# Optimization experiments

Measured on AMD Instinct MI355X. Metric: run time of the kernel, lower is better.

The kernel has to match this reference:

```python
import jax, jax.numpy as jnp
import numpy as np

N = 100000
E = 1600000
IN_F = 128
OUT_F = 64
NEG_SLOPE = 0.2


def setup_inputs() -> dict:
    key = jax.random.key(0)
    k1, k2, k3, k4 = jax.random.split(key, 4)
    h = jax.random.normal(k1, (N, IN_F), dtype=jnp.float32)
    edge_index = jax.random.randint(k2, (2, E), 0, N, dtype=jnp.int64 if jax.config.jax_enable_x64 else jnp.int32)
    # glorot-initialized params (scale ~ sqrt(6/(fan_in+fan_out)))
    ws = float(np.sqrt(6.0 / (IN_F + OUT_F)))
    W = jax.random.uniform(k3, (OUT_F, IN_F), dtype=jnp.float32, minval=-ws, maxval=ws)
    as_ = float(np.sqrt(6.0 / (1 + 2 * OUT_F)))
    a = jax.random.uniform(k4, (1, 2 * OUT_F), dtype=jnp.float32, minval=-as_, maxval=as_)
    return {"h": h, "W": W, "a": a, "edge_index": edge_index}


def reference(h, W, a, edge_index):
    n = h.shape[0]
    f_out = W.shape[0]
    h_lin = h @ W.T  # [N, F_out]
    # add self loops
    loops = jnp.arange(n, dtype=edge_index.dtype)
    row = jnp.concatenate([edge_index[0], loops])  # [E+N]
    col = jnp.concatenate([edge_index[1], loops])
    # cat([h_lin[row], h_lin[col]]) @ a.T == h_lin[row]@a1 + h_lin[col]@a2
    a1 = a[0, :f_out]
    a2 = a[0, f_out:]
    s_src = h_lin @ a1  # [N]
    s_dst = h_lin @ a2  # [N]
    e = s_src[row] + s_dst[col]  # [E+N]
    e = jnp.where(e > 0, e, NEG_SLOPE * e)  # LeakyReLU
    # segment softmax over destination (row); every row appears via self loop
    m = jax.ops.segment_max(e, row, num_segments=n)
    ex = jnp.exp(e - m[row])
    denom = jax.ops.segment_sum(ex, row, num_segments=n)
    alpha = ex / denom[row]
    # scatter-add aggregation
    h_prime = jax.ops.segment_sum(alpha[:, None] * h_lin[col], row, num_segments=n)
    return jax.nn.elu(h_prime)
```

## Files before the change

### kernel.cpp

```cpp
#include <hip/hip_runtime.h>
#include <cstdint>

#define N_NODES 100000
#define E_EDGES 1600000
#define TOTAL_E (E_EDGES + N_NODES)
#define IN_F 128
#define OUT_F 64
#define NEG_SLOPE 0.2f

#define NB   256
#define RPB  391
#define GCAP 8192
#define TILE 4096
#define EPT  (TILE / 256)
#define HALF_R 196
#define CCAP 4608

typedef __attribute__((ext_vector_type(8))) short short8;
typedef __attribute__((ext_vector_type(4))) float float4v;

__device__ __forceinline__ short bf16_rne(float x) {
  unsigned u = __builtin_bit_cast(unsigned, x);
  unsigned r = u + 0x7FFFu + ((u >> 16) & 1u);
  return (short)(r >> 16);
}
__device__ __forceinline__ float bf16_f(short s) {
  unsigned u = ((unsigned)(unsigned short)s) << 16;
  return __builtin_bit_cast(float, u);
}
__device__ __forceinline__ float bf16u_f(unsigned short s) {
  unsigned u = ((unsigned)s) << 16;
  return __builtin_bit_cast(float, u);
}

__global__ __launch_bounds__(256) void k_linear(
    const float* __restrict__ h, const float* __restrict__ W,
    const float* __restrict__ a, unsigned short* __restrict__ h_lin,
    float* __restrict__ s_src, float* __restrict__ s_dst) {
  __shared__ alignas(16) short Whi[16 * 512];
  __shared__ alignas(16) short Wlo[16 * 512];

  const int tid = threadIdx.x;
  for (int i = tid; i < OUT_F * IN_F; i += 256) {
    const int n = i >> 7, k = i & 127;
    const float x = W[i];
    const short hi = bf16_rne(x);
    const short lo = bf16_rne(x - bf16_f(hi));
    const int idx = (((k >> 5) * 4 + (n >> 4)) << 9) |
                    (((((k >> 3) & 3) << 4) | (n & 15)) << 3) | (k & 7);
    Whi[idx] = hi;
    Wlo[idx] = lo;
  }
  __syncthreads();

  const int lane = tid & 63;
  const int m    = lane & 15;
  const int q    = lane >> 4;
  const int wgid = blockIdx.x * 4 + (tid >> 6);
  const int nw   = gridDim.x * 4;

  float a1v[4], a2v[4];
#pragma unroll
  for (int t = 0; t < 4; ++t) {
    a1v[t] = a[t * 16 + m];
    a2v[t] = a[OUT_F + t * 16 + m];
  }

  for (int tile = wgid; tile < N_NODES / 16; tile += nw) {
    const int row0 = tile * 16;
    float4v acc[4] = {{0.f,0.f,0.f,0.f},{0.f,0.f,0.f,0.f},
                      {0.f,0.f,0.f,0.f},{0.f,0.f,0.f,0.f}};

    const float* hbase = h + (size_t)(row0 + m) * IN_F + q * 8;
#pragma unroll
    for (int ks = 0; ks < 4; ++ks) {
      const float4 f0 = *(const float4*)(hbase + 32 * ks);
      const float4 f1 = *(const float4*)(hbase + 32 * ks + 4);
      float av[8] = {f0.x, f0.y, f0.z, f0.w, f1.x, f1.y, f1.z, f1.w};
      short8 ahi, alo;
#pragma unroll
      for (int j = 0; j < 8; ++j) {
        const short hi = bf16_rne(av[j]);
        ahi[j] = hi;
        alo[j] = bf16_rne(av[j] - bf16_f(hi));
      }
#pragma unroll
      for (int t = 0; t < 4; ++t) {
        const int fb = ((ks * 4 + t) << 9) + lane * 8;
        const short8 bhi = *(const short8*)&Whi[fb];
        const short8 blo = *(const short8*)&Wlo[fb];
        acc[t] = __builtin_amdgcn_mfma_f32_16x16x32_bf16(ahi, bhi, acc[t], 0, 0, 0);
        acc[t] = __builtin_amdgcn_mfma_f32_16x16x32_bf16(ahi, blo, acc[t], 0, 0, 0);
        acc[t] = __builtin_amdgcn_mfma_f32_16x16x32_bf16(alo, bhi, acc[t], 0, 0, 0);
      }
    }

#pragma unroll
    for (int t = 0; t < 4; ++t)
#pragma unroll
      for (int r = 0; r < 4; ++r)
        h_lin[(size_t)(row0 + q * 4 + r) * OUT_F + t * 16 + m] =
            (unsigned short)bf16_rne(acc[t][r]);

#pragma unroll
    for (int r = 0; r < 4; ++r) {
      float p = acc[0][r] * a1v[0] + acc[1][r] * a1v[1] +
                acc[2][r] * a1v[2] + acc[3][r] * a1v[3];
      float qq = acc[0][r] * a2v[0] + acc[1][r] * a2v[1] +
                 acc[2][r] * a2v[2] + acc[3][r] * a2v[3];
#pragma unroll
      for (int o = 1; o < 16; o <<= 1) {
        p  += __shfl_xor(p, o, 64);
        qq += __shfl_xor(qq, o, 64);
      }
      if (m == 0) {
        s_src[row0 + q * 4 + r] = p;
        s_dst[row0 + q * 4 + r] = qq;
      }
    }
  }
}

__global__ __launch_bounds__(256) void k_bin(
    const int* __restrict__ ei, int* __restrict__ gcur,
    unsigned* __restrict__ regions) {
  __shared__ unsigned reord[TILE];
  __shared__ unsigned char bktid[TILE];
  __shared__ int hist[NB];
  __shared__ int scan_s[NB];
  __shared__ int adj[NB];
  __shared__ int wsum[4];

  const int tid = threadIdx.x;
  const int e0  = blockIdx.x * TILE;

  hist[tid] = 0;
  __syncthreads();

  int      myb[EPT];
  unsigned myrec[EPT];
#pragma unroll
  for (int k = 0; k < EPT; ++k) {
    const int e = e0 + k * 256 + tid;
    int b = -1; unsigned rec = 0;
    if (e < TOTAL_E) {
      int r, c;
      if (e < E_EDGES) { r = ei[e]; c = ei[E_EDGES + e]; }
      else             { r = e - E_EDGES; c = r; }
      b = (int)((unsigned)r / RPB);
      rec = ((unsigned)(r - b * RPB) << 17) | (unsigned)c;
      atomicAdd(&hist[b], 1);
    }
    myb[k] = b; myrec[k] = rec;
  }
  __syncthreads();

  const int lane = tid & 63, w = tid >> 6;
  {
    const int v = hist[tid];
    int incl = v;
#pragma unroll
    for (int o = 1; o < 64; o <<= 1) {
      const int t = __shfl_up(incl, o, 64);
      if (lane >= o) incl += t;
    }
    if (lane == 63) wsum[w] = incl;
    __syncthreads();
    int wpre = 0;
    for (int i = 0; i < w; ++i) wpre += wsum[i];
    scan_s[tid] = wpre + incl - v;
    adj[tid]    = wpre + incl - v;
  }
  __syncthreads();

#pragma unroll
  for (int k = 0; k < EPT; ++k) {
    if (myb[k] >= 0) {
      const int pos = atomicAdd(&adj[myb[k]], 1);
      reord[pos]  = myrec[k];
      bktid[pos]  = (unsigned char)myb[k];
    }
  }
  __syncthreads();

  {
    const int cnt = hist[tid];
    int a2 = 0;
    if (cnt > 0) a2 = atomicAdd(&gcur[tid], cnt) - scan_s[tid];
    __syncthreads();
    adj[tid] = a2;
  }
  __syncthreads();

  const int tilesz = scan_s[NB - 1] + hist[NB - 1];
  for (int i = tid; i < tilesz; i += 256) {
    const int b    = bktid[i];
    const int slot = adj[b] + i;
    if (slot < GCAP) regions[(size_t)b * GCAP + slot] = reord[i];
  }
}

__global__ __launch_bounds__(1024) void k_agg(
    const unsigned short* __restrict__ h_lin, const float* __restrict__ s_src,
    const float* __restrict__ s_dst, const int* __restrict__ gcur,
    const unsigned* __restrict__ regions, float* __restrict__ out) {
  __shared__ int cnt[HALF_R];
  __shared__ int off[HALF_R];
  __shared__ int cols[CCAP];
  __shared__ int wsum4[4];

  const int blk  = blockIdx.x;
  const int b    = blk >> 1;
  const int half = blk & 1;
  const int rlo  = half * HALF_R;
  const int hr   = half ? (RPB - HALF_R) : HALF_R;
  const int tid  = threadIdx.x;
  const int row0 = b * RPB + rlo;
  const int m    = min(gcur[b], GCAP);
  const unsigned* reg = regions + (size_t)b * GCAP;

  for (int i = tid; i < HALF_R; i += 1024) cnt[i] = 0;
  __syncthreads();

  unsigned myrec[GCAP / 1024];
  int nmy = 0;
  for (int i = tid; i < m; i += 1024) {
    const unsigned rec = reg[i];
    const int rl = (int)(rec >> 17) - rlo;
    if (rl >= 0 && rl < hr) {
      myrec[nmy++] = rec;
      atomicAdd(&cnt[rl], 1);
    }
  }
  __syncthreads();

  const int lane = tid & 63, wv = tid >> 6;
  int incl = 0, v = 0;
  if (tid < 256) {
    v = (tid < hr) ? cnt[tid] : 0;
    incl = v;
#pragma unroll
    for (int o = 1; o < 64; o <<= 1) {
      const int t = __shfl_up(incl, o, 64);
      if (lane >= o) incl += t;
    }
    if (lane == 63) wsum4[wv] = incl;
  }
  __syncthreads();
  if (tid < hr) {
    int wpre = 0;
    for (int i = 0; i < wv; ++i) wpre += wsum4[i];
    off[tid] = wpre + incl - v;
  }
  __syncthreads();

  for (int k = 0; k < nmy; ++k) {
    const unsigned rec = myrec[k];
    const int rl  = (int)(rec >> 17) - rlo;
    const int pos = atomicAdd(&off[rl], 1);
    if (pos < CCAP) cols[pos] = (int)(rec & 0x1FFFFu);
  }
  __syncthreads();

  for (int rl = wv; rl < hr; rl += 16) {
    const int row = row0 + rl;
    if (row >= N_NODES) break;
    const int dcnt  = cnt[rl];
    const int end   = off[rl];
    const int start = end - dcnt;
    const int deg   = min(dcnt, 64);
    const float s1 = s_src[row];

    int c = 0;
    if (lane < deg) c = cols[start + lane];
    float e = s1 + ((lane < deg) ? s_dst[c] : 0.f);
    e = e > 0.f ? e : NEG_SLOPE * e;
    const float ex = __expf(e);

    float acc = 0.f, dsum = 0.f;
    int j = 0;
    for (; j + 4 <= deg; j += 4) {
      const int   c0 = __shfl(c, j, 64),      c1 = __shfl(c, j + 1, 64);
      const int   c2 = __shfl(c, j + 2, 64),  c3 = __shfl(c, j + 3, 64);
      const float e0 = __shfl(ex, j, 64),     e1 = __shfl(ex, j + 1, 64);
      const float e2 = __shfl(ex, j + 2, 64), e3 = __shfl(ex, j + 3, 64);
      const float v0 = bf16u_f(h_lin[(size_t)c0 * OUT_F + lane]);
      const float v1 = bf16u_f(h_lin[(size_t)c1 * OUT_F + lane]);
      const float v2 = bf16u_f(h_lin[(size_t)c2 * OUT_F + lane]);
      const float v3 = bf16u_f(h_lin[(size_t)c3 * OUT_F + lane]);
      acc = fmaf(e0, v0, acc); acc = fmaf(e1, v1, acc);
      acc = fmaf(e2, v2, acc); acc = fmaf(e3, v3, acc);
      dsum += (e0 + e1) + (e2 + e3);
    }
    for (; j < deg; ++j) {
      const int   cj = __shfl(c, j, 64);
      const float ej = __shfl(ex, j, 64);
      acc = fmaf(ej, bf16u_f(h_lin[(size_t)cj * OUT_F + lane]), acc);
      dsum += ej;
    }

    const float hp = acc / dsum;
    out[(size_t)row * OUT_F + lane] = hp > 0.f ? hp : __expf(hp) - 1.f;
  }
}

extern "C" void kernel_launch(void* const* d_in, const int* in_sizes, int n_in,
                              void* d_out, int out_size, void* d_ws, size_t ws_size,
                              hipStream_t stream) {
  const float* h  = (const float*)d_in[0];
  const float* W  = (const float*)d_in[1];
  const float* a  = (const float*)d_in[2];
  const int*   ei = (const int*)d_in[3];
  float* out = (float*)d_out;

  unsigned short* h_lin = (unsigned short*)d_ws;
  float* s_src = (float*)(h_lin + (size_t)N_NODES * OUT_F);
  float* s_dst = s_src + N_NODES;
  int*   gcur  = (int*)(s_dst + N_NODES);
  unsigned* regions = (unsigned*)(gcur + NB);

  hipMemsetAsync(gcur, 0, NB * sizeof(int), stream);

  k_linear<<<782, 256, 0, stream>>>(h, W, a, h_lin, s_src, s_dst);

  k_bin<<<(TOTAL_E + TILE - 1) / TILE, 256, 0, stream>>>(ei, gcur, regions);

  k_agg<<<NB * 2, 1024, 0, stream>>>(h_lin, s_src, s_dst, gcur, regions, out);
}
```

Measured before the change: 188.9 us.

## Precompute edge attention weights during bucketing and gather two features per lane

The aggregation kernel now computes each edge's exp score while scattering edges into per-row slots. It stores (col, weight) pairs in shared memory, which removes the per-row shuffle broadcast and the 64-degree cap. In the gather loop each wave splits into two half-waves that process alternating edges, and each lane loads two bf16 features as one 32-bit word; the halves are combined with a cross-lane xor shuffle. This costs double the LDS footprint for the pairs array and a second pass over the global edge records instead of caching them in registers.

New measurement: 182.9 us. 3.2% less time.

```diff
diff --git a/kernel.cpp b/kernel.cpp
--- a/kernel.cpp
+++ b/kernel.cpp
@@ -26,10 +26,6 @@
 }
 __device__ __forceinline__ float bf16_f(short s) {
   unsigned u = ((unsigned)(unsigned short)s) << 16;
-  return __builtin_bit_cast(float, u);
-}
-__device__ __forceinline__ float bf16u_f(unsigned short s) {
-  unsigned u = ((unsigned)s) << 16;
   return __builtin_bit_cast(float, u);
 }
 
@@ -204,10 +200,11 @@
     const unsigned short* __restrict__ h_lin, const float* __restrict__ s_src,
     const float* __restrict__ s_dst, const int* __restrict__ gcur,
     const unsigned* __restrict__ regions, float* __restrict__ out) {
-  __shared__ int cnt[HALF_R];
-  __shared__ int off[HALF_R];
-  __shared__ int cols[CCAP];
-  __shared__ int wsum4[4];
+  __shared__ int   cnt[HALF_R];
+  __shared__ int   off[HALF_R];
+  __shared__ float srcs[HALF_R];
+  __shared__ uint2 pairs[CCAP];
+  __shared__ int   wsum4[4];
 
   const int blk  = blockIdx.x;
   const int b    = blk >> 1;
@@ -219,18 +216,15 @@
   const int m    = min(gcur[b], GCAP);
   const unsigned* reg = regions + (size_t)b * GCAP;
 
-  for (int i = tid; i < HALF_R; i += 1024) cnt[i] = 0;
-  __syncthreads();
-
-  unsigned myrec[GCAP / 1024];
-  int nmy = 0;
+  for (int i = tid; i < HALF_R; i += 1024) {
+    cnt[i]  = 0;
+    srcs[i] = (i < hr && row0 + i < N_NODES) ? s_src[row0 + i] : 0.f;
+  }
+  __syncthreads();
+
   for (int i = tid; i < m; i += 1024) {
-    const unsigned rec = reg[i];
-    const int rl = (int)(rec >> 17) - rlo;
-    if (rl >= 0 && rl < hr) {
-      myrec[nmy++] = rec;
-      atomicAdd(&cnt[rl], 1);
-    }
+    const int rl = (int)(reg[i] >> 17) - rlo;
+    if (rl >= 0 && rl < hr) atomicAdd(&cnt[rl], 1);
   }
   __syncthreads();
 
@@ -254,53 +248,63 @@
   }
   __syncthreads();
 
-  for (int k = 0; k < nmy; ++k) {
-    const unsigned rec = myrec[k];
-    const int rl  = (int)(rec >> 17) - rlo;
-    const int pos = atomicAdd(&off[rl], 1);
-    if (pos < CCAP) cols[pos] = (int)(rec & 0x1FFFFu);
-  }
-  __syncthreads();
-
+  for (int i = tid; i < m; i += 1024) {
+    const unsigned rec = reg[i];
+    const int rl = (int)(rec >> 17) - rlo;
+    if (rl >= 0 && rl < hr) {
+      const int c = (int)(rec & 0x1FFFFu);
+      float e = srcs[rl] + s_dst[c];
+      e = e > 0.f ? e : NEG_SLOPE * e;
+      const float ex = __expf(e);
+      const int pos = atomicAdd(&off[rl], 1);
+      if (pos < CCAP) pairs[pos] = make_uint2((unsigned)c, __float_as_uint(ex));
+    }
+  }
+  __syncthreads();
+
+  const int hid = lane >> 5;
+  const int fl  = (lane & 31) * 2;
   for (int rl = wv; rl < hr; rl += 16) {
     const int row = row0 + rl;
     if (row >= N_NODES) break;
     const int dcnt  = cnt[rl];
     const int end   = off[rl];
     const int start = end - dcnt;
-    const int deg   = min(dcnt, 64);
-    const float s1 = s_src[row];
-
-    int c = 0;
-    if (lane < deg) c = cols[start + lane];
-    float e = s1 + ((lane < deg) ? s_dst[c] : 0.f);
-    e = e > 0.f ? e : NEG_SLOPE * e;
-    const float ex = __expf(e);
-
-    float acc = 0.f, dsum = 0.f;
-    int j = 0;
-    for (; j + 4 <= deg; j += 4) {
-      const int   c0 = __shfl(c, j, 64),      c1 = __shfl(c, j + 1, 64);
-      const int   c2 = __shfl(c, j + 2, 64),  c3 = __shfl(c, j + 3, 64);
-      const float e0 = __shfl(ex, j, 64),     e1 = __shfl(ex, j + 1, 64);
-      const float e2 = __shfl(ex, j + 2, 64), e3 = __shfl(ex, j + 3, 64);
-      const float v0 = bf16u_f(h_lin[(size_t)c0 * OUT_F + lane]);
-      const float v1 = bf16u_f(h_lin[(size_t)c1 * OUT_F + lane]);
-      const float v2 = bf16u_f(h_lin[(size_t)c2 * OUT_F + lane]);
-      const float v3 = bf16u_f(h_lin[(size_t)c3 * OUT_F + lane]);
-      acc = fmaf(e0, v0, acc); acc = fmaf(e1, v1, acc);
-      acc = fmaf(e2, v2, acc); acc = fmaf(e3, v3, acc);
-      dsum += (e0 + e1) + (e2 + e3);
-    }
-    for (; j < deg; ++j) {
-      const int   cj = __shfl(c, j, 64);
-      const float ej = __shfl(ex, j, 64);
-      acc = fmaf(ej, bf16u_f(h_lin[(size_t)cj * OUT_F + lane]), acc);
-      dsum += ej;
-    }
-
-    const float hp = acc / dsum;
-    out[(size_t)row * OUT_F + lane] = hp > 0.f ? hp : __expf(hp) - 1.f;
+
+    float accx = 0.f, accy = 0.f, dsum = 0.f;
+    int j = hid;
+    for (; j + 2 < dcnt; j += 4) {
+      const uint2 p0 = pairs[start + j];
+      const uint2 p1 = pairs[start + j + 2];
+      const unsigned h0 = *(const unsigned*)&h_lin[(size_t)p0.x * OUT_F + fl];
+      const unsigned h1 = *(const unsigned*)&h_lin[(size_t)p1.x * OUT_F + fl];
+      const float e0 = __uint_as_float(p0.y);
+      const float e1 = __uint_as_float(p1.y);
+      accx = fmaf(e0, __builtin_bit_cast(float, h0 << 16), accx);
+      accy = fmaf(e0, __builtin_bit_cast(float, h0 & 0xFFFF0000u), accy);
+      accx = fmaf(e1, __builtin_bit_cast(float, h1 << 16), accx);
+      accy = fmaf(e1, __builtin_bit_cast(float, h1 & 0xFFFF0000u), accy);
+      dsum += e0 + e1;
+    }
+    if (j < dcnt) {
+      const uint2 p0 = pairs[start + j];
+      const unsigned h0 = *(const unsigned*)&h_lin[(size_t)p0.x * OUT_F + fl];
+      const float e0 = __uint_as_float(p0.y);
+      accx = fmaf(e0, __builtin_bit_cast(float, h0 << 16), accx);
+      accy = fmaf(e0, __builtin_bit_cast(float, h0 & 0xFFFF0000u), accy);
+      dsum += e0;
+    }
+
+    accx += __shfl_xor(accx, 32, 64);
+    accy += __shfl_xor(accy, 32, 64);
+    dsum += __shfl_xor(dsum, 32, 64);
+
+    if (lane < 32) {
+      float hx = accx / dsum, hy = accy / dsum;
+      hx = hx > 0.f ? hx : __expf(hx) - 1.f;
+      hy = hy > 0.f ? hy : __expf(hy) - 1.f;
+      *(float2*)&out[(size_t)row * OUT_F + fl] = make_float2(hx, hy);
+    }
   }
 }
 
```
